# Kernel optimization log

Measured on AMD Instinct MI355X. Metric: run time of the kernel, lower is better.

Reference implementation:

```python
import jax, jax.numpy as jnp
import numpy as np

OUT_FEATURES = 8192
PACKED_IN = 4096          # in_features = 2 * PACKED_IN = 8192
GROUP_SIZE = 128
N_GROUPS = (2 * PACKED_IN) // GROUP_SIZE  # 64


def _unpack_int4(packed):
    """Unpack bytes (stored as int32 in [0,256)) into signed int4 pairs [O, 2P].

    Matches torch: high nibble first, then low nibble, both sign-corrected
    (values >= 8 map to value - 16).
    """
    high = packed >> 4
    low = packed & 15
    high = jnp.where(high >= 8, high - 16, high)
    low = jnp.where(low >= 8, low - 16, low)
    return jnp.stack([high, low], axis=-1).reshape(packed.shape[0], -1)


def setup_inputs() -> dict:
    key = jax.random.key(0)
    k1, k2, k3, k4, k5 = jax.random.split(key, 5)
    x = jax.random.normal(k1, (1, 128, 2 * PACKED_IN), dtype=jnp.float32)
    weight_q = jax.random.randint(k2, (OUT_FEATURES, PACKED_IN), 0, 256, dtype=jnp.int32)
    # small positive per-group scales, float zero points (as in the torch module)
    scale = jax.random.uniform(k3, (OUT_FEATURES, N_GROUPS), dtype=jnp.float32) * 0.05 + 1e-3
    zero_point = jax.random.normal(k4, (OUT_FEATURES, N_GROUPS), dtype=jnp.float32)
    bias = jax.random.normal(k5, (OUT_FEATURES,), dtype=jnp.float32)
    return {"x": x, "weight_q": weight_q, "scale": scale, "zero_point": zero_point, "bias": bias}


def reference(x, weight_q, scale, zero_point, bias):
    O = weight_q.shape[0]
    w = _unpack_int4(weight_q).astype(jnp.float32)          # [O, in]
    wg = w.reshape(O, N_GROUPS, GROUP_SIZE)                  # group view
    # (w - zp) * scale, broadcast per group (== repeat_interleave in torch)
    W = ((wg - zero_point[:, :, None]) * scale[:, :, None]).reshape(O, -1)
    return jnp.einsum('bsi,oi->bso', x, W) + bias
```

## Files before the change

kernel.cpp:

```cpp
#include <hip/hip_runtime.h>
#include <hip/hip_bf16.h>
#include <stdint.h>

#define M_DIM 128
#define N_DIM 8192
#define K_DIM 8192
#define KP    4096
#define NGRP  64
#define KSPLIT 8
#define KCHUNK (K_DIM / KSPLIT)
#define BK    64
#define NSTEPS (KCHUNK / BK)

typedef __attribute__((ext_vector_type(8))) short bf16x8;
typedef __attribute__((ext_vector_type(4))) float f32x4;

__device__ __forceinline__ unsigned short f2bf(float f) {
  unsigned int u = __float_as_uint(f);
  return (unsigned short)((u + 0x7fffu + ((u >> 16) & 1u)) >> 16);
}

__global__ void xcast_kernel(const float* __restrict__ x, unsigned short* __restrict__ xb) {
  int idx = (blockIdx.x * blockDim.x + threadIdx.x) * 8;
  const float4* xp = (const float4*)(x + idx);
  float4 a = xp[0], b = xp[1];
  uint4 o;
  o.x = (unsigned)f2bf(a.x) | ((unsigned)f2bf(a.y) << 16);
  o.y = (unsigned)f2bf(a.z) | ((unsigned)f2bf(a.w) << 16);
  o.z = (unsigned)f2bf(b.x) | ((unsigned)f2bf(b.y) << 16);
  o.w = (unsigned)f2bf(b.z) | ((unsigned)f2bf(b.w) << 16);
  *(uint4*)(xb + idx) = o;
}

__global__ __launch_bounds__(256, 2)
void gemm_kernel(const unsigned short* __restrict__ xb,
                 const int* __restrict__ wq,
                 const float* __restrict__ scale,
                 const float* __restrict__ zpt,
                 unsigned short* __restrict__ partial)
{
  __shared__ uint4 xtile[2][1024];
  __shared__ uint4 wtile[2][1024];

  const int tid = threadIdx.x;
  const int l   = tid & 63;
  const int w   = tid >> 6;
  const int l15 = l & 15;
  const int lk  = l >> 4;
  const int n0  = blockIdx.x * 128;
  const int ks  = blockIdx.y;
  const int k0  = ks * KCHUNK;

  const int r0 = n0 + w * 32 + l15;
  const int r1 = r0 + 16;

  const float* sp0 = scale + r0 * NGRP + ks * 8;
  const float* zp0 = zpt   + r0 * NGRP + ks * 8;
  const float* sp1 = scale + r1 * NGRP + ks * 8;
  const float* zp1 = zpt   + r1 * NGRP + ks * 8;
  float4 s0a = *(const float4*)sp0,     s0b = *(const float4*)(sp0 + 4);
  float4 z0a = *(const float4*)zp0,     z0b = *(const float4*)(zp0 + 4);
  float4 s1a = *(const float4*)sp1,     s1b = *(const float4*)(sp1 + 4);
  float4 z1a = *(const float4*)zp1,     z1b = *(const float4*)(zp1 + 4);

  auto STAGE = [&](int t, int nb) {
    const int kt = k0 + t * BK;
    #pragma unroll
    for (int i = 0; i < 4; ++i) {
      int c = i * 256 + tid;
      int row = c >> 3, q = (c & 7) ^ (row & 7);
      const unsigned short* src = xb + (size_t)row * K_DIM + kt + q * 8;
      uint4* dst = &xtile[nb][i * 256 + w * 64];
      __builtin_amdgcn_global_load_lds(
          (__attribute__((address_space(1))) void*)(void*)src,
          (__attribute__((address_space(3))) void*)(void*)dst, 16, 0, 0);
    }
    #pragma unroll
    for (int i = 0; i < 4; ++i) {
      int c = i * 256 + tid;
      int row = c >> 3, q = (c & 7) ^ (row & 7);
      const int* src = wq + (size_t)(n0 + row) * KP + (k0 >> 1) + t * 32 + q * 4;
      uint4* dst = &wtile[nb][i * 256 + w * 64];
      __builtin_amdgcn_global_load_lds(
          (__attribute__((address_space(1))) void*)(void*)src,
          (__attribute__((address_space(3))) void*)(void*)dst, 16, 0, 0);
    }
  };

  f32x4 acc[8][2];
  #pragma unroll
  for (int mi = 0; mi < 8; ++mi)
    #pragma unroll
    for (int ni = 0; ni < 2; ++ni) {
      f32x4 z = {0.f, 0.f, 0.f, 0.f};
      acc[mi][ni] = z;
    }

  STAGE(0, 0);
  STAGE(1, 1);
  float scs0[8] = {s0a.x, s0a.y, s0a.z, s0a.w, s0b.x, s0b.y, s0b.z, s0b.w};
  float scs1[8] = {s1a.x, s1a.y, s1a.z, s1a.w, s1b.x, s1b.y, s1b.z, s1b.w};
  float nzs0[8] = {-z0a.x * s0a.x, -z0a.y * s0a.y, -z0a.z * s0a.z, -z0a.w * s0a.w,
                   -z0b.x * s0b.x, -z0b.y * s0b.y, -z0b.z * s0b.z, -z0b.w * s0b.w};
  float nzs1[8] = {-z1a.x * s1a.x, -z1a.y * s1a.y, -z1a.z * s1a.z, -z1a.w * s1a.w,
                   -z1b.x * s1b.x, -z1b.y * s1b.y, -z1b.z * s1b.z, -z1b.w * s1b.w};

  const int wrow0 = w * 32 + l15;
  const int wrow1 = wrow0 + 16;

  #pragma unroll
  for (int t = 0; t < NSTEPS; ++t) {
    asm volatile("s_waitcnt vmcnt(8)" ::: "memory");
    __builtin_amdgcn_s_barrier();

    const int cb = t & 1;
    const float sc[2] = {scs0[t >> 1], scs1[t >> 1]};
    const float nz[2] = {nzs0[t >> 1], nzs1[t >> 1]};

    #pragma unroll
    for (int kk = 0; kk < 2; ++kk) {
      const int q = kk * 4 + lk;
      uint4 av[8];
      #pragma unroll
      for (int mi = 0; mi < 8; ++mi) {
        int r = mi * 16 + l15;
        av[mi] = xtile[cb][r * 8 + (q ^ (r & 7))];
      }
      uint4 pw[2];
      pw[0] = wtile[cb][wrow0 * 8 + (q ^ (wrow0 & 7))];
      pw[1] = wtile[cb][wrow1 * 8 + (q ^ (wrow1 & 7))];
      uint4 bq[2];
      #pragma unroll
      for (int ni = 0; ni < 2; ++ni) {
        int v4[4] = {(int)pw[ni].x, (int)pw[ni].y, (int)pw[ni].z, (int)pw[ni].w};
        unsigned words[4];
        #pragma unroll
        for (int j = 0; j < 4; ++j) {
          int hi = (v4[j] << 24) >> 28;
          int lo = (v4[j] << 28) >> 28;
          float fh = fmaf((float)hi, sc[ni], nz[ni]);
          float fl = fmaf((float)lo, sc[ni], nz[ni]);
          asm("v_cvt_pk_bf16_f32 %0, %1, %2" : "=v"(words[j]) : "v"(fh), "v"(fl));
        }
        uint4 o; o.x = words[0]; o.y = words[1]; o.z = words[2]; o.w = words[3];
        bq[ni] = o;
      }
      #pragma unroll
      for (int mi = 0; mi < 8; ++mi)
        #pragma unroll
        for (int ni = 0; ni < 2; ++ni)
          acc[mi][ni] = __builtin_amdgcn_mfma_f32_16x16x32_bf16(
              __builtin_bit_cast(bf16x8, av[mi]),
              __builtin_bit_cast(bf16x8, bq[ni]),
              acc[mi][ni], 0, 0, 0);
    }

    __builtin_amdgcn_s_barrier();
    STAGE(t + 2 < NSTEPS ? t + 2 : NSTEPS - 1, t & 1);
  }
  asm volatile("s_waitcnt vmcnt(0)" ::: "memory");

  unsigned short* p = partial + (size_t)ks * (M_DIM * N_DIM);
  #pragma unroll
  for (int mi = 0; mi < 8; ++mi)
    #pragma unroll
    for (int ni = 0; ni < 2; ++ni) {
      int col = n0 + w * 32 + ni * 16 + l15;
      int rowb = mi * 16 + lk * 4;
      #pragma unroll
      for (int j = 0; j < 4; ++j)
        p[(size_t)(rowb + j) * N_DIM + col] = f2bf(acc[mi][ni][j]);
    }
}

__global__ void reduce_kernel(const unsigned short* __restrict__ part,
                              const float* __restrict__ bias,
                              float* __restrict__ out) {
  int idx = (blockIdx.x * blockDim.x + threadIdx.x) * 8;
  float s[8];
  #pragma unroll
  for (int j = 0; j < 8; ++j) s[j] = 0.f;
  #pragma unroll
  for (int k = 0; k < KSPLIT; ++k) {
    uint4 v = *(const uint4*)(part + (size_t)k * (M_DIM * N_DIM) + idx);
    unsigned ws[4] = {v.x, v.y, v.z, v.w};
    #pragma unroll
    for (int j = 0; j < 4; ++j) {
      s[2 * j]     += __uint_as_float((ws[j] & 0xffffu) << 16);
      s[2 * j + 1] += __uint_as_float(ws[j] & 0xffff0000u);
    }
  }
  int col = idx & (N_DIM - 1);
  float4 b0 = *(const float4*)(bias + col);
  float4 b1 = *(const float4*)(bias + col + 4);
  float4 o0, o1;
  o0.x = s[0] + b0.x; o0.y = s[1] + b0.y; o0.z = s[2] + b0.z; o0.w = s[3] + b0.w;
  o1.x = s[4] + b1.x; o1.y = s[5] + b1.y; o1.z = s[6] + b1.z; o1.w = s[7] + b1.w;
  *(float4*)(out + idx) = o0;
  *(float4*)(out + idx + 4) = o1;
}

extern "C" void kernel_launch(void* const* d_in, const int* in_sizes, int n_in,
                              void* d_out, int out_size, void* d_ws, size_t ws_size,
                              hipStream_t stream) {
  const float* x     = (const float*)d_in[0];
  const int*   wq    = (const int*)d_in[1];
  const float* scale = (const float*)d_in[2];
  const float* zpt   = (const float*)d_in[3];
  const float* bias  = (const float*)d_in[4];
  float* out = (float*)d_out;

  unsigned short* xb = (unsigned short*)d_ws;
  const size_t xbytes = (size_t)M_DIM * K_DIM * 2;
  unsigned short* partial = (unsigned short*)((char*)d_ws + xbytes);

  xcast_kernel<<<(M_DIM * K_DIM) / (256 * 8), 256, 0, stream>>>(x, xb);
  gemm_kernel<<<dim3(N_DIM / 128, KSPLIT), 256, 0, stream>>>(
      xb, wq, scale, zpt, partial);
  reduce_kernel<<<(M_DIM * N_DIM) / (256 * 8), 256, 0, stream>>>(
      partial, bias, out);
}
```

Measured before the change: 44.51 us.

## Replace split-K partial buffer and reduce kernel with float atomic adds

Bias initialisation of the output moves into the x-cast kernel, and the GEMM kernel accumulates its split-K partial results straight into the output with float atomicAdd. This drops the bf16 partial buffer and the separate reduce launch, saving a kernel launch plus the write and re-read of eight partial planes. In exchange there are 8-way contended scalar atomics on every output element. The summation order also becomes nondeterministic, although partials now stay in fp32 instead of being rounded to bf16.

```diff
diff --git a/kernel.cpp b/kernel.cpp
--- a/kernel.cpp
+++ b/kernel.cpp
@@ -20,7 +20,8 @@
   return (unsigned short)((u + 0x7fffu + ((u >> 16) & 1u)) >> 16);
 }
 
-__global__ void xcast_kernel(const float* __restrict__ x, unsigned short* __restrict__ xb) {
+__global__ void xcast_kernel(const float* __restrict__ x, unsigned short* __restrict__ xb,
+                             const float* __restrict__ bias, float* __restrict__ out) {
   int idx = (blockIdx.x * blockDim.x + threadIdx.x) * 8;
   const float4* xp = (const float4*)(x + idx);
   float4 a = xp[0], b = xp[1];
@@ -30,6 +31,11 @@
   o.z = (unsigned)f2bf(b.x) | ((unsigned)f2bf(b.y) << 16);
   o.w = (unsigned)f2bf(b.z) | ((unsigned)f2bf(b.w) << 16);
   *(uint4*)(xb + idx) = o;
+  int col = idx & (N_DIM - 1);
+  float4 b0 = *(const float4*)(bias + col);
+  float4 b1 = *(const float4*)(bias + col + 4);
+  *(float4*)(out + idx) = b0;
+  *(float4*)(out + idx + 4) = b1;
 }
 
 __global__ __launch_bounds__(256, 2)
@@ -37,7 +43,7 @@
                  const int* __restrict__ wq,
                  const float* __restrict__ scale,
                  const float* __restrict__ zpt,
-                 unsigned short* __restrict__ partial)
+                 float* __restrict__ out)
 {
   __shared__ uint4 xtile[2][1024];
   __shared__ uint4 wtile[2][1024];
@@ -160,7 +166,6 @@
   }
   asm volatile("s_waitcnt vmcnt(0)" ::: "memory");
 
-  unsigned short* p = partial + (size_t)ks * (M_DIM * N_DIM);
   #pragma unroll
   for (int mi = 0; mi < 8; ++mi)
     #pragma unroll
@@ -169,35 +174,8 @@
       int rowb = mi * 16 + lk * 4;
       #pragma unroll
       for (int j = 0; j < 4; ++j)
-        p[(size_t)(rowb + j) * N_DIM + col] = f2bf(acc[mi][ni][j]);
+        atomicAdd(out + (size_t)(rowb + j) * N_DIM + col, acc[mi][ni][j]);
     }
-}
-
-__global__ void reduce_kernel(const unsigned short* __restrict__ part,
-                              const float* __restrict__ bias,
-                              float* __restrict__ out) {
-  int idx = (blockIdx.x * blockDim.x + threadIdx.x) * 8;
-  float s[8];
-  #pragma unroll
-  for (int j = 0; j < 8; ++j) s[j] = 0.f;
-  #pragma unroll
-  for (int k = 0; k < KSPLIT; ++k) {
-    uint4 v = *(const uint4*)(part + (size_t)k * (M_DIM * N_DIM) + idx);
-    unsigned ws[4] = {v.x, v.y, v.z, v.w};
-    #pragma unroll
-    for (int j = 0; j < 4; ++j) {
-      s[2 * j]     += __uint_as_float((ws[j] & 0xffffu) << 16);
-      s[2 * j + 1] += __uint_as_float(ws[j] & 0xffff0000u);
-    }
-  }
-  int col = idx & (N_DIM - 1);
-  float4 b0 = *(const float4*)(bias + col);
-  float4 b1 = *(const float4*)(bias + col + 4);
-  float4 o0, o1;
-  o0.x = s[0] + b0.x; o0.y = s[1] + b0.y; o0.z = s[2] + b0.z; o0.w = s[3] + b0.w;
-  o1.x = s[4] + b1.x; o1.y = s[5] + b1.y; o1.z = s[6] + b1.z; o1.w = s[7] + b1.w;
-  *(float4*)(out + idx) = o0;
-  *(float4*)(out + idx + 4) = o1;
 }
 
 extern "C" void kernel_launch(void* const* d_in, const int* in_sizes, int n_in,
@@ -211,12 +189,8 @@
   float* out = (float*)d_out;
 
   unsigned short* xb = (unsigned short*)d_ws;
-  const size_t xbytes = (size_t)M_DIM * K_DIM * 2;
-  unsigned short* partial = (unsigned short*)((char*)d_ws + xbytes);
 
-  xcast_kernel<<<(M_DIM * K_DIM) / (256 * 8), 256, 0, stream>>>(x, xb);
+  xcast_kernel<<<(M_DIM * K_DIM) / (256 * 8), 256, 0, stream>>>(x, xb, bias, out);
   gemm_kernel<<<dim3(N_DIM / 128, KSPLIT), 256, 0, stream>>>(
-      xb, wq, scale, zpt, partial);
-  reduce_kernel<<<(M_DIM * N_DIM) / (256 * 8), 256, 0, stream>>>(
-      partial, bias, out);
+      xb, wq, scale, zpt, out);
 }
```

Result: slower. 57.90 us (+30.1%).

## Transpose split-K partial layout for vectorized stores and LDS-transposed reduce

Applied to the files above, without the earlier changes.

The GEMM epilogue now writes partial sums in an N-major [o][s] layout, so each lane packs four accumulator values into one 8-byte store instead of four scattered 2-byte stores. The reduce kernel reads this transposed layout and adds the bias per output feature. It then transposes through a shared-memory tile to write the M-major output with float4 stores. The goal is to cut uncoalesced narrow stores in the GEMM epilogue, at the cost of an LDS round trip and a barrier in the reduce.

```diff
diff --git a/kernel.cpp b/kernel.cpp
--- a/kernel.cpp
+++ b/kernel.cpp
@@ -160,29 +160,38 @@
   }
   asm volatile("s_waitcnt vmcnt(0)" ::: "memory");
 
-  unsigned short* p = partial + (size_t)ks * (M_DIM * N_DIM);
+  unsigned short* p = partial + (size_t)ks * (N_DIM * M_DIM);
   #pragma unroll
   for (int mi = 0; mi < 8; ++mi)
     #pragma unroll
     for (int ni = 0; ni < 2; ++ni) {
-      int col = n0 + w * 32 + ni * 16 + l15;
-      int rowb = mi * 16 + lk * 4;
-      #pragma unroll
-      for (int j = 0; j < 4; ++j)
-        p[(size_t)(rowb + j) * N_DIM + col] = f2bf(acc[mi][ni][j]);
+      int o  = n0 + w * 32 + ni * 16 + l15;
+      int sb = mi * 16 + lk * 4;
+      f32x4 v = acc[mi][ni];
+      unsigned w0, w1;
+      asm("v_cvt_pk_bf16_f32 %0, %1, %2" : "=v"(w0) : "v"(v[0]), "v"(v[1]));
+      asm("v_cvt_pk_bf16_f32 %0, %1, %2" : "=v"(w1) : "v"(v[2]), "v"(v[3]));
+      uint2 st; st.x = w0; st.y = w1;
+      *(uint2*)(p + (size_t)o * M_DIM + sb) = st;
     }
 }
 
 __global__ void reduce_kernel(const unsigned short* __restrict__ part,
                               const float* __restrict__ bias,
                               float* __restrict__ out) {
-  int idx = (blockIdx.x * blockDim.x + threadIdx.x) * 8;
+  __shared__ float tile[16][132];
+  const int t = threadIdx.x;
+  const int o_loc = t >> 4;
+  const int sg    = t & 15;
+  const int o  = blockIdx.x * 16 + o_loc;
+  const int s0 = sg * 8;
+
   float s[8];
   #pragma unroll
   for (int j = 0; j < 8; ++j) s[j] = 0.f;
   #pragma unroll
   for (int k = 0; k < KSPLIT; ++k) {
-    uint4 v = *(const uint4*)(part + (size_t)k * (M_DIM * N_DIM) + idx);
+    uint4 v = *(const uint4*)(part + (size_t)k * (N_DIM * M_DIM) + (size_t)o * M_DIM + s0);
     unsigned ws[4] = {v.x, v.y, v.z, v.w};
     #pragma unroll
     for (int j = 0; j < 4; ++j) {
@@ -190,14 +199,23 @@
       s[2 * j + 1] += __uint_as_float(ws[j] & 0xffff0000u);
     }
   }
-  int col = idx & (N_DIM - 1);
-  float4 b0 = *(const float4*)(bias + col);
-  float4 b1 = *(const float4*)(bias + col + 4);
-  float4 o0, o1;
-  o0.x = s[0] + b0.x; o0.y = s[1] + b0.y; o0.z = s[2] + b0.z; o0.w = s[3] + b0.w;
-  o1.x = s[4] + b1.x; o1.y = s[5] + b1.y; o1.z = s[6] + b1.z; o1.w = s[7] + b1.w;
-  *(float4*)(out + idx) = o0;
-  *(float4*)(out + idx + 4) = o1;
+  const float b = bias[o];
+  #pragma unroll
+  for (int j = 0; j < 8; ++j) tile[o_loc][s0 + j] = s[j] + b;
+  __syncthreads();
+
+  const int o4 = (t & 3) * 4;
+  const int sr = t >> 2;
+  #pragma unroll
+  for (int rep = 0; rep < 2; ++rep) {
+    int srow = sr + rep * 64;
+    float4 ov;
+    ov.x = tile[o4 + 0][srow];
+    ov.y = tile[o4 + 1][srow];
+    ov.z = tile[o4 + 2][srow];
+    ov.w = tile[o4 + 3][srow];
+    *(float4*)(out + (size_t)srow * N_DIM + blockIdx.x * 16 + o4) = ov;
+  }
 }
 
 extern "C" void kernel_launch(void* const* d_in, const int* in_sizes, int n_in,
@@ -217,6 +235,5 @@
   xcast_kernel<<<(M_DIM * K_DIM) / (256 * 8), 256, 0, stream>>>(x, xb);
   gemm_kernel<<<dim3(N_DIM / 128, KSPLIT), 256, 0, stream>>>(
       xb, wq, scale, zpt, partial);
-  reduce_kernel<<<(M_DIM * N_DIM) / (256 * 8), 256, 0, stream>>>(
-      partial, bias, out);
-}
+  reduce_kernel<<<N_DIM / 16, 256, 0, stream>>>(partial, bias, out);
+}
```

Measured after the change: 46.45 us. 4.3% more time.
